# Kernel tuning notes

Measured on AMD Instinct MI355X. Metric: run time of the kernel, lower is better.

Reference implementation:

```python
import jax, jax.numpy as jnp
import numpy as np

IN_FEATURES = 3072
OUT_FEATURES = 4096
PADDED = 4096  # 2**ceil(log2(in_features))
PADDING = PADDED - IN_FEATURES
MIN_RANGE = -384.0
MAX_RANGE = 384.0
Q_LEVELS = 255.0  # 8-bit affine quantization


def fwht(x):
    """Unnormalized fast Walsh-Hadamard transform along the last axis.
    H @ H = n * I, matching the /padded_dim rescale in forward."""
    n = x.shape[-1]
    m = int(round(np.log2(n)))
    lead = x.shape[:-1]
    x = x.reshape((-1,) + (2,) * m)
    for ax in range(1, m + 1):  # m <= 12 fixed butterfly stages
        a = jnp.take(x, 0, axis=ax)
        b = jnp.take(x, 1, axis=ax)
        x = jnp.stack([a + b, a - b], axis=ax)
    return x.reshape(lead + (n,))


def quant_dequant(x):
    """QuantizedMatrix: clip to [MIN_RANGE, MAX_RANGE], 8-bit affine
    quantize, then dequantize (reference computes the dequantized values)."""
    scale = (MAX_RANGE - MIN_RANGE) / Q_LEVELS
    q = jnp.clip(jnp.round((jnp.clip(x, MIN_RANGE, MAX_RANGE) - MIN_RANGE) / scale), 0.0, Q_LEVELS)
    return q * scale + MIN_RANGE


def setup_inputs() -> dict:
    key = jax.random.key(0)
    k1, k2, k3 = jax.random.split(key, 3)
    x = jax.random.normal(k1, (2, 4096, IN_FEATURES), dtype=jnp.float32)
    weight = jax.random.normal(k2, (OUT_FEATURES, IN_FEATURES), dtype=jnp.float32)
    bias = jax.random.normal(k3, (OUT_FEATURES,), dtype=jnp.float32)
    return {"x": x, "weight": weight, "bias": bias}


def reference(x, weight, bias):
    # pad feature dim to power of two, Hadamard-rotate activations and weights
    xh = fwht(jnp.pad(x, ((0, 0), (0, 0), (0, PADDING))))          # [B,S,P]
    wh = fwht(jnp.pad(weight, ((0, 0), (0, PADDING))))              # [O,P]
    qx = quant_dequant(xh)
    qw = quant_dequant(wh)
    # qx @ qw / padded_dim + bias  (qw contracted over the padded dim)
    return jnp.einsum('bsp,op->bso', qx, qw) / PADDED + bias
```

## Files before the change

kernel.cpp:

```cpp
#include <hip/hip_runtime.h>

typedef int v4i __attribute__((ext_vector_type(4)));
typedef int v16i __attribute__((ext_vector_type(16)));

#define IN_F   3072
#define PAD    4096
#define M_ROWS 8192
#define N_OUT  4096

#define BM 128
#define BN 256
#define BK 64

__device__ __forceinline__ void async_copy16(const void* g, void* l) {
    __builtin_amdgcn_global_load_lds(
        (__attribute__((address_space(1))) const void*)(uintptr_t)g,
        (__attribute__((address_space(3))) void*)(uint32_t)(uintptr_t)l,
        16, 0, 0);
}

__device__ __forceinline__ void fwht16(float v[16]) {
#pragma unroll
    for (int s = 1; s < 16; s <<= 1) {
#pragma unroll
        for (int i = 0; i < 16; i++) {
            if ((i & s) == 0) {
                float a = v[i], b = v[i ^ s];
                v[i]     = a + b;
                v[i ^ s] = a - b;
            }
        }
    }
}

__global__ __launch_bounds__(256) void fwht_quant_kernel(
    const float* __restrict__ in, signed char* __restrict__ qout,
    int* __restrict__ rowsum, int nrows)
{
    __shared__ float lds[4096];
    __shared__ int ssum;
    const int t = threadIdx.x;
    const int r = blockIdx.x;
    if (r >= nrows) return;
    const float* row = in + (size_t)r * IN_F;

    float v[16];
#pragma unroll
    for (int j = 0; j < 16; j++)
        v[j] = (j < 12) ? row[j * 256 + t] : 0.0f;

    fwht16(v);

    const int th = t >> 4, tl = t & 15;

    #pragma unroll
    for (int j = 0; j < 16; j++)
        lds[256 * j + 16 * (th ^ j) + (tl ^ th)] = v[j];
    __syncthreads();
#pragma unroll
    for (int j = 0; j < 16; j++)
        v[j] = lds[256 * th + 16 * (j ^ th) + (tl ^ j)];

    fwht16(v);

    if (t == 0) ssum = 0;
    __syncthreads();

#pragma unroll
    for (int j = 0; j < 16; j++)
        lds[256 * th + 16 * (j ^ th) + (tl ^ j)] = v[j];
    __syncthreads();
#pragma unroll
    for (int j = 0; j < 16; j++)
        v[j] = lds[256 * th + 16 * (tl ^ th) + (j ^ tl)];

    fwht16(v);

    const float INV = 0.33203125f;
    int sum = 0;
    int pk[4];
#pragma unroll
    for (int c = 0; c < 4; c++) {
        int word = 0;
#pragma unroll
        for (int b = 0; b < 4; b++) {
            float x = v[c * 4 + b];
            x = fminf(fmaxf(x, -384.0f), 384.0f);
            float qf = rintf((x + 384.0f) * INV);
            int qi = (int)qf;
            qi = qi < 0 ? 0 : (qi > 255 ? 255 : qi);
            int a = qi - 128;
            sum += a;
            word |= (a & 255) << (8 * b);
        }
        pk[c] = word;
    }

#pragma unroll
    for (int off = 32; off > 0; off >>= 1) sum += __shfl_down(sum, off, 64);
    if ((t & 63) == 0) atomicAdd(&ssum, sum);

    ((int4*)(qout + (size_t)r * PAD))[t] = make_int4(pk[0], pk[1], pk[2], pk[3]);

    __syncthreads();
    if (t == 0) rowsum[r] = ssum;
}

__global__ __launch_bounds__(256, 2) void gemm_i8_kernel(
    const signed char* __restrict__ A, const signed char* __restrict__ B,
    const int* __restrict__ SA, const int* __restrict__ SB,
    const float* __restrict__ bias, float* __restrict__ out,
    float kA, float kS, float kC)
{
    __shared__ __align__(16) signed char As[BM * BK];
    __shared__ __align__(16) signed char Bs[BN * BK];

    const int tid  = threadIdx.x;
    const int lane = tid & 63;
    const int wid  = tid >> 6;
    const int wr   = wid >> 1, wc = wid & 1;
    const int bm   = blockIdx.y * BM;
    const int bn   = blockIdx.x * BN;
    const int l5   = lane >> 5;
    const int lm   = lane & 31;

    v16i acc[2][4];
#pragma unroll
    for (int i = 0; i < 2; i++)
#pragma unroll
        for (int j = 0; j < 4; j++)
#pragma unroll
            for (int e = 0; e < 16; e++)
                acc[i][j][e] = 0;

    for (int bk = 0; bk < PAD; bk += BK) {
#pragma unroll
        for (int i = 0; i < 2; i++) {
            int c = wid * 128 + i * 64 + lane;
            int rr = c >> 2, p = c & 3;
            int q = (p - rr) & 3;
            async_copy16(A + (size_t)(bm + rr) * PAD + bk + q * 16,
                         As + (wid * 128 + i * 64) * 16);
        }
#pragma unroll
        for (int i = 0; i < 4; i++) {
            int c = wid * 256 + i * 64 + lane;
            int rr = c >> 2, p = c & 3;
            int q = (p - rr) & 3;
            async_copy16(B + (size_t)(bn + rr) * PAD + bk + q * 16,
                         Bs + (wid * 256 + i * 64) * 16);
        }
        __syncthreads();

#pragma unroll
        for (int ks = 0; ks < 2; ks++) {
            const int qbase = ks * 2 + l5;
            v4i a[2], b[4];
#pragma unroll
            for (int mt = 0; mt < 2; mt++) {
                int rr = wr * 64 + mt * 32 + lm;
                int p = (qbase + rr) & 3;
                a[mt] = *(const v4i*)(As + rr * 64 + p * 16);
            }
#pragma unroll
            for (int nt = 0; nt < 4; nt++) {
                int rr = wc * 128 + nt * 32 + lm;
                int p = (qbase + rr) & 3;
                b[nt] = *(const v4i*)(Bs + rr * 64 + p * 16);
            }
#pragma unroll
            for (int mt = 0; mt < 2; mt++)
#pragma unroll
                for (int nt = 0; nt < 4; nt++)
                    acc[mt][nt] = __builtin_amdgcn_mfma_i32_32x32x32_i8(
                        a[mt], b[nt], acc[mt][nt], 0, 0, 0);
        }
        __syncthreads();
    }

#pragma unroll
    for (int nt = 0; nt < 4; nt++) {
        int n = bn + wc * 128 + nt * 32 + lm;
        float ct = (float)SB[n] * kS + kC + bias[n];
#pragma unroll
        for (int mt = 0; mt < 2; mt++) {
#pragma unroll
            for (int e = 0; e < 16; e++) {
                int m = bm + wr * 64 + mt * 32 + l5 * 4 + (e & 3) + 8 * (e >> 2);
                out[(size_t)m * N_OUT + n] =
                    (float)acc[mt][nt][e] * kA + (float)SA[m] * kS + ct;
            }
        }
    }
}

extern "C" void kernel_launch(void* const* d_in, const int* in_sizes, int n_in,
                              void* d_out, int out_size, void* d_ws, size_t ws_size,
                              hipStream_t stream) {
    const float* x    = (const float*)d_in[0];
    const float* w    = (const float*)d_in[1];
    const float* bias = (const float*)d_in[2];
    float* out = (float*)d_out;

    signed char* qa = (signed char*)d_ws;
    signed char* qb = qa + (size_t)M_ROWS * PAD;
    int* SA = (int*)(qb + (size_t)N_OUT * PAD);
    int* SB = SA + M_ROWS;

    fwht_quant_kernel<<<M_ROWS, 256, 0, stream>>>(x, qa, SA, M_ROWS);
    fwht_quant_kernel<<<N_OUT,  256, 0, stream>>>(w, qb, SB, N_OUT);

    double s = 768.0 / 255.0;
    double c = 384.0 / 255.0;
    float kA = (float)(s * s / PAD);
    float kS = (float)(s * c / PAD);
    float kC = (float)(c * c);

    dim3 grid(N_OUT / BN, M_ROWS / BM);
    gemm_i8_kernel<<<grid, 256, 0, stream>>>(qa, qb, SA, SB, bias, out, kA, kS, kC);
}
```

Measured before the change: 399.2 us.

## Triple-buffer int8 GEMM LDS tiles with async prefetch and MFMA priority

Replaces the single-buffered load-sync-compute loop in the int8 GEMM with a three-stage LDS ring, so tiles are prefetched two iterations ahead and overlap with MFMA work. Partial vmcnt waits replace the full syncthreads drains. It also changes the LDS swizzle to rotate by row pair instead of row to alter bank-conflict patterns, and raises wave priority around the MFMA block. LDS use triples (to 72KB per block), which may limit occupancy below the requested two blocks per CU.

```diff
diff --git a/kernel.cpp b/kernel.cpp
--- a/kernel.cpp
+++ b/kernel.cpp
@@ -112,8 +112,8 @@
     const float* __restrict__ bias, float* __restrict__ out,
     float kA, float kS, float kC)
 {
-    __shared__ __align__(16) signed char As[BM * BK];
-    __shared__ __align__(16) signed char Bs[BN * BK];
+    __shared__ __align__(16) signed char As[3][BM * BK];
+    __shared__ __align__(16) signed char Bs[3][BN * BK];
 
     const int tid  = threadIdx.x;
     const int lane = tid & 63;
@@ -133,49 +133,75 @@
             for (int e = 0; e < 16; e++)
                 acc[i][j][e] = 0;
 
-    for (int bk = 0; bk < PAD; bk += BK) {
+    auto stage = [&](int b, int kt) {
+        const int bk = kt * BK;
 #pragma unroll
         for (int i = 0; i < 2; i++) {
             int c = wid * 128 + i * 64 + lane;
             int rr = c >> 2, p = c & 3;
-            int q = (p - rr) & 3;
+            int q = (p - (rr >> 1)) & 3;
             async_copy16(A + (size_t)(bm + rr) * PAD + bk + q * 16,
-                         As + (wid * 128 + i * 64) * 16);
+                         As[b] + (wid * 128 + i * 64) * 16);
         }
 #pragma unroll
         for (int i = 0; i < 4; i++) {
             int c = wid * 256 + i * 64 + lane;
             int rr = c >> 2, p = c & 3;
-            int q = (p - rr) & 3;
+            int q = (p - (rr >> 1)) & 3;
             async_copy16(B + (size_t)(bn + rr) * PAD + bk + q * 16,
-                         Bs + (wid * 256 + i * 64) * 16);
-        }
-        __syncthreads();
-
+                         Bs[b] + (wid * 256 + i * 64) * 16);
+        }
+    };
+
+    auto compute = [&](int b) {
 #pragma unroll
         for (int ks = 0; ks < 2; ks++) {
             const int qbase = ks * 2 + l5;
-            v4i a[2], b[4];
+            v4i af[2], bf[4];
 #pragma unroll
             for (int mt = 0; mt < 2; mt++) {
                 int rr = wr * 64 + mt * 32 + lm;
-                int p = (qbase + rr) & 3;
-                a[mt] = *(const v4i*)(As + rr * 64 + p * 16);
+                int p = (qbase + (rr >> 1)) & 3;
+                af[mt] = *(const v4i*)(As[b] + rr * 64 + p * 16);
             }
 #pragma unroll
             for (int nt = 0; nt < 4; nt++) {
                 int rr = wc * 128 + nt * 32 + lm;
-                int p = (qbase + rr) & 3;
-                b[nt] = *(const v4i*)(Bs + rr * 64 + p * 16);
-            }
+                int p = (qbase + (rr >> 1)) & 3;
+                bf[nt] = *(const v4i*)(Bs[b] + rr * 64 + p * 16);
+            }
+            __builtin_amdgcn_s_setprio(1);
 #pragma unroll
             for (int mt = 0; mt < 2; mt++)
 #pragma unroll
                 for (int nt = 0; nt < 4; nt++)
                     acc[mt][nt] = __builtin_amdgcn_mfma_i32_32x32x32_i8(
-                        a[mt], b[nt], acc[mt][nt], 0, 0, 0);
-        }
-        __syncthreads();
+                        af[mt], bf[nt], acc[mt][nt], 0, 0, 0);
+            __builtin_amdgcn_s_setprio(0);
+        }
+    };
+
+    constexpr int T = PAD / BK;
+
+    stage(0, 0);
+    stage(1, 1);
+    asm volatile("s_waitcnt vmcnt(6)" ::: "memory");
+    __builtin_amdgcn_s_barrier();
+    asm volatile("" ::: "memory");
+
+    int b0 = 0, b1 = 1, b2 = 2;
+    for (int t = 0; t < T; ++t) {
+        if (t + 2 < T) stage(b2, t + 2);
+        compute(b0);
+        if (t < T - 1) {
+            if (t + 2 < T)
+                asm volatile("s_waitcnt vmcnt(6)" ::: "memory");
+            else
+                asm volatile("s_waitcnt vmcnt(0)" ::: "memory");
+            __builtin_amdgcn_s_barrier();
+            asm volatile("" ::: "memory");
+        }
+        int tmp = b0; b0 = b1; b1 = b2; b2 = tmp;
     }
 
 #pragma unroll
```

Result: no change. 393.4 us (-1.4%).

## Restructure int8 GEMM with 256x256 tiles, triple-buffered LDS pipeline and block swizzle

Applied to the files above, without the earlier changes.

The int8 GEMM now uses 512-thread blocks computing 256x256 output tiles. Global-to-LDS async copies are triple-buffered with prefetch two tiles ahead and interleaved between MFMA groups, with explicit vmcnt waits and raw barriers in place of syncthreads. It also remaps the 1D block index for L2 locality, precomputes LDS offsets with a new swizzle, and raises MFMA priority with setprio. The aim is to hide global load latency and improve data reuse, at the cost of more LDS (96KB) and registers per block, which may limit occupancy.

```diff
diff --git a/kernel.cpp b/kernel.cpp
--- a/kernel.cpp
+++ b/kernel.cpp
@@ -8,9 +8,11 @@
 #define M_ROWS 8192
 #define N_OUT  4096
 
-#define BM 128
+#define BM 256
 #define BN 256
 #define BK 64
+#define TBUF (BM * BK)
+#define TTILES (PAD / BK)
 
 __device__ __forceinline__ void async_copy16(const void* g, void* l) {
     __builtin_amdgcn_global_load_lds(
@@ -106,87 +108,166 @@
     if (t == 0) rowsum[r] = ssum;
 }
 
-__global__ __launch_bounds__(256, 2) void gemm_i8_kernel(
+__global__ __launch_bounds__(512, 2) void gemm_i8_kernel(
     const signed char* __restrict__ A, const signed char* __restrict__ B,
     const int* __restrict__ SA, const int* __restrict__ SB,
     const float* __restrict__ bias, float* __restrict__ out,
     float kA, float kS, float kC)
 {
-    __shared__ __align__(16) signed char As[BM * BK];
-    __shared__ __align__(16) signed char Bs[BN * BK];
+    __shared__ __align__(16) signed char As[3 * TBUF];
+    __shared__ __align__(16) signed char Bs[3 * TBUF];
 
     const int tid  = threadIdx.x;
     const int lane = tid & 63;
     const int wid  = tid >> 6;
-    const int wr   = wid >> 1, wc = wid & 1;
-    const int bm   = blockIdx.y * BM;
-    const int bn   = blockIdx.x * BN;
+    const int wr   = wid >> 2;
+    const int wc   = wid & 3;
     const int l5   = lane >> 5;
     const int lm   = lane & 31;
 
-    v16i acc[2][4];
-#pragma unroll
-    for (int i = 0; i < 2; i++)
-#pragma unroll
-        for (int j = 0; j < 4; j++)
+    const int bid = (int)blockIdx.x;
+    const int swz = ((bid & 7) << 6) | (bid >> 3);
+    const int bm  = (swz >> 4) * BM;
+    const int bn  = (swz & 15) * BN;
+
+    v16i acc[4][2];
+#pragma unroll
+    for (int i = 0; i < 4; i++)
+#pragma unroll
+        for (int j = 0; j < 2; j++)
 #pragma unroll
             for (int e = 0; e < 16; e++)
                 acc[i][j][e] = 0;
 
-    for (int bk = 0; bk < PAD; bk += BK) {
-#pragma unroll
-        for (int i = 0; i < 2; i++) {
-            int c = wid * 128 + i * 64 + lane;
-            int rr = c >> 2, p = c & 3;
-            int q = (p - rr) & 3;
-            async_copy16(A + (size_t)(bm + rr) * PAD + bk + q * 16,
-                         As + (wid * 128 + i * 64) * 16);
-        }
-#pragma unroll
-        for (int i = 0; i < 4; i++) {
-            int c = wid * 256 + i * 64 + lane;
-            int rr = c >> 2, p = c & 3;
-            int q = (p - rr) & 3;
-            async_copy16(B + (size_t)(bn + rr) * PAD + bk + q * 16,
-                         Bs + (wid * 256 + i * 64) * 16);
-        }
-        __syncthreads();
-
+    const signed char* srcA[2];
+    const signed char* srcB[2];
+    int dstO[2];
+#pragma unroll
+    for (int i = 0; i < 2; i++) {
+        int c  = wid * 128 + i * 64 + lane;
+        int rr = c >> 2, p = c & 3;
+        int q  = (p - (rr >> 1)) & 3;
+        srcA[i] = A + (size_t)(bm + rr) * PAD + q * 16;
+        srcB[i] = B + (size_t)(bn + rr) * PAD + q * 16;
+        dstO[i] = (wid * 128 + i * 64) * 16;
+    }
+
+    int aoff[4][2], boff[2][2];
+#pragma unroll
+    for (int mt = 0; mt < 4; mt++) {
+        int rr = wr * 128 + mt * 32 + lm;
 #pragma unroll
         for (int ks = 0; ks < 2; ks++) {
-            const int qbase = ks * 2 + l5;
-            v4i a[2], b[4];
-#pragma unroll
-            for (int mt = 0; mt < 2; mt++) {
-                int rr = wr * 64 + mt * 32 + lm;
-                int p = (qbase + rr) & 3;
-                a[mt] = *(const v4i*)(As + rr * 64 + p * 16);
+            int p = (ks * 2 + l5 + (rr >> 1)) & 3;
+            aoff[mt][ks] = rr * 64 + p * 16;
+        }
+    }
+#pragma unroll
+    for (int nt = 0; nt < 2; nt++) {
+        int rr = wc * 64 + nt * 32 + lm;
+#pragma unroll
+        for (int ks = 0; ks < 2; ks++) {
+            int p = (ks * 2 + l5 + (rr >> 1)) & 3;
+            boff[nt][ks] = rr * 64 + p * 16;
+        }
+    }
+
+#pragma unroll
+    for (int i = 0; i < 2; i++) async_copy16(srcA[i],      As + dstO[i]);
+#pragma unroll
+    for (int i = 0; i < 2; i++) async_copy16(srcB[i],      Bs + dstO[i]);
+#pragma unroll
+    for (int i = 0; i < 2; i++) async_copy16(srcA[i] + BK, As + TBUF + dstO[i]);
+#pragma unroll
+    for (int i = 0; i < 2; i++) async_copy16(srcB[i] + BK, Bs + TBUF + dstO[i]);
+    asm volatile("s_waitcnt vmcnt(4)" ::: "memory");
+    __builtin_amdgcn_s_barrier();
+    asm volatile("" ::: "memory");
+
+    int ob0 = 0, ob1 = TBUF, ob2 = 2 * TBUF;
+
+    for (int t = 0; t < TTILES; ++t) {
+        const signed char* Ab = As + ob0;
+        const signed char* Bb = Bs + ob0;
+        const int  pk = (t + 2) * BK;
+        const bool pf = (t + 2 < TTILES);
+
+        v4i bfr[2][2];
+#pragma unroll
+        for (int nt = 0; nt < 2; nt++)
+#pragma unroll
+            for (int ks = 0; ks < 2; ks++)
+                bfr[nt][ks] = *(const v4i*)(Bb + boff[nt][ks]);
+
+        {
+            v4i x0 = *(const v4i*)(Ab + aoff[0][0]);
+            v4i x1 = *(const v4i*)(Ab + aoff[0][1]);
+            if (pf) async_copy16(srcA[0] + pk, As + ob2 + dstO[0]);
+            __builtin_amdgcn_s_setprio(1);
+            acc[0][0] = __builtin_amdgcn_mfma_i32_32x32x32_i8(x0, bfr[0][0], acc[0][0], 0, 0, 0);
+            acc[0][1] = __builtin_amdgcn_mfma_i32_32x32x32_i8(x0, bfr[1][0], acc[0][1], 0, 0, 0);
+            acc[0][0] = __builtin_amdgcn_mfma_i32_32x32x32_i8(x1, bfr[0][1], acc[0][0], 0, 0, 0);
+            acc[0][1] = __builtin_amdgcn_mfma_i32_32x32x32_i8(x1, bfr[1][1], acc[0][1], 0, 0, 0);
+            __builtin_amdgcn_s_setprio(0);
+            __builtin_amdgcn_s_barrier();
+            asm volatile("" ::: "memory");
+        }
+        {
+            v4i x0 = *(const v4i*)(Ab + aoff[1][0]);
+            v4i x1 = *(const v4i*)(Ab + aoff[1][1]);
+            if (pf) async_copy16(srcA[1] + pk, As + ob2 + dstO[1]);
+            __builtin_amdgcn_s_setprio(1);
+            acc[1][0] = __builtin_amdgcn_mfma_i32_32x32x32_i8(x0, bfr[0][0], acc[1][0], 0, 0, 0);
+            acc[1][1] = __builtin_amdgcn_mfma_i32_32x32x32_i8(x0, bfr[1][0], acc[1][1], 0, 0, 0);
+            acc[1][0] = __builtin_amdgcn_mfma_i32_32x32x32_i8(x1, bfr[0][1], acc[1][0], 0, 0, 0);
+            acc[1][1] = __builtin_amdgcn_mfma_i32_32x32x32_i8(x1, bfr[1][1], acc[1][1], 0, 0, 0);
+            __builtin_amdgcn_s_setprio(0);
+            __builtin_amdgcn_s_barrier();
+            asm volatile("" ::: "memory");
+        }
+        {
+            v4i x0 = *(const v4i*)(Ab + aoff[2][0]);
+            v4i x1 = *(const v4i*)(Ab + aoff[2][1]);
+            if (pf) async_copy16(srcB[0] + pk, Bs + ob2 + dstO[0]);
+            __builtin_amdgcn_s_setprio(1);
+            acc[2][0] = __builtin_amdgcn_mfma_i32_32x32x32_i8(x0, bfr[0][0], acc[2][0], 0, 0, 0);
+            acc[2][1] = __builtin_amdgcn_mfma_i32_32x32x32_i8(x0, bfr[1][0], acc[2][1], 0, 0, 0);
+            acc[2][0] = __builtin_amdgcn_mfma_i32_32x32x32_i8(x1, bfr[0][1], acc[2][0], 0, 0, 0);
+            acc[2][1] = __builtin_amdgcn_mfma_i32_32x32x32_i8(x1, bfr[1][1], acc[2][1], 0, 0, 0);
+            __builtin_amdgcn_s_setprio(0);
+            __builtin_amdgcn_s_barrier();
+            asm volatile("" ::: "memory");
+        }
+        {
+            v4i x0 = *(const v4i*)(Ab + aoff[3][0]);
+            v4i x1 = *(const v4i*)(Ab + aoff[3][1]);
+            if (pf) async_copy16(srcB[1] + pk, Bs + ob2 + dstO[1]);
+            __builtin_amdgcn_s_setprio(1);
+            acc[3][0] = __builtin_amdgcn_mfma_i32_32x32x32_i8(x0, bfr[0][0], acc[3][0], 0, 0, 0);
+            acc[3][1] = __builtin_amdgcn_mfma_i32_32x32x32_i8(x0, bfr[1][0], acc[3][1], 0, 0, 0);
+            acc[3][0] = __builtin_amdgcn_mfma_i32_32x32x32_i8(x1, bfr[0][1], acc[3][0], 0, 0, 0);
+            acc[3][1] = __builtin_amdgcn_mfma_i32_32x32x32_i8(x1, bfr[1][1], acc[3][1], 0, 0, 0);
+            __builtin_amdgcn_s_setprio(0);
+            if (t < TTILES - 1) {
+                if (pf) asm volatile("s_waitcnt vmcnt(4)" ::: "memory");
+                else    asm volatile("s_waitcnt vmcnt(0)" ::: "memory");
+                __builtin_amdgcn_s_barrier();
+                asm volatile("" ::: "memory");
             }
-#pragma unroll
-            for (int nt = 0; nt < 4; nt++) {
-                int rr = wc * 128 + nt * 32 + lm;
-                int p = (qbase + rr) & 3;
-                b[nt] = *(const v4i*)(Bs + rr * 64 + p * 16);
-            }
-#pragma unroll
-            for (int mt = 0; mt < 2; mt++)
-#pragma unroll
-                for (int nt = 0; nt < 4; nt++)
-                    acc[mt][nt] = __builtin_amdgcn_mfma_i32_32x32x32_i8(
-                        a[mt], b[nt], acc[mt][nt], 0, 0, 0);
-        }
-        __syncthreads();
-    }
-
-#pragma unroll
-    for (int nt = 0; nt < 4; nt++) {
-        int n = bn + wc * 128 + nt * 32 + lm;
+        }
+
+        int tmp = ob0; ob0 = ob1; ob1 = ob2; ob2 = tmp;
+    }
+
+#pragma unroll
+    for (int nt = 0; nt < 2; nt++) {
+        int n = bn + wc * 64 + nt * 32 + lm;
         float ct = (float)SB[n] * kS + kC + bias[n];
 #pragma unroll
-        for (int mt = 0; mt < 2; mt++) {
+        for (int mt = 0; mt < 4; mt++) {
 #pragma unroll
             for (int e = 0; e < 16; e++) {
-                int m = bm + wr * 64 + mt * 32 + l5 * 4 + (e & 3) + 8 * (e >> 2);
+                int m = bm + wr * 128 + mt * 32 + l5 * 4 + (e & 3) + 8 * (e >> 2);
                 out[(size_t)m * N_OUT + n] =
                     (float)acc[mt][nt][e] * kA + (float)SA[m] * kS + ct;
             }
@@ -216,6 +297,6 @@
     float kS = (float)(s * c / PAD);
     float kC = (float)(c * c);
 
-    dim3 grid(N_OUT / BN, M_ROWS / BM);
-    gemm_i8_kernel<<<grid, 256, 0, stream>>>(qa, qb, SA, SB, bias, out, kA, kS, kC);
-}
+    dim3 grid((M_ROWS / BM) * (N_OUT / BN));
+    gemm_i8_kernel<<<grid, 512, 0, stream>>>(qa, qb, SA, SB, bias, out, kA, kS, kC);
+}
```

Result: faster. 373.5 us (-6.4%).
